# Kernel tuning notes

Measured on AMD Instinct MI355X. Metric: run time of the kernel, lower is better.

The kernel has to match this reference:

```python
import jax, jax.numpy as jnp
import numpy as np

B, HQ, HKV, D = 32, 32, 8, 128
PAGE = 16           # page_size == kv_seq_blk_size
PPS = 256           # pages per sequence -> 4096-token KV context
NPAGES = B * PPS


def setup_inputs() -> dict:
    key = jax.random.key(0)
    k1, k2, k3, k4 = jax.random.split(key, 4)
    q = jax.random.normal(k1, (B, HQ, 1, D), dtype=jnp.float32)
    paged_kv_cache = jax.random.normal(k2, (NPAGES, 2, HKV, PAGE, D), dtype=jnp.float32)
    # Uniform pages-per-sequence CSR layout; pages scattered randomly in the pool.
    kv_page_indptr = (jnp.arange(B + 1, dtype=jnp.int32) * PPS)
    kv_page_indices = jax.random.permutation(k3, NPAGES).astype(jnp.int32)
    kv_last_page_len = jax.random.randint(k4, (B,), 1, PAGE + 1, dtype=jnp.int32)
    return {
        "q": q,
        "paged_kv_cache": paged_kv_cache,
        "kv_page_indptr": kv_page_indptr,
        "kv_page_indices": kv_page_indices,
        "kv_last_page_len": kv_last_page_len,
    }


def reference(q, paged_kv_cache, kv_page_indptr, kv_page_indices, kv_last_page_len):
    b, hq, _, d = q.shape
    hkv = paged_kv_cache.shape[2]
    page = paged_kv_cache.shape[3]
    pps = kv_page_indices.shape[0] // b          # uniform pages per sequence
    groups = hq // hkv
    scale = 1.0 / jnp.sqrt(jnp.asarray(d, dtype=q.dtype))

    # Gather each sequence's pages: [B, PPS] page ids -> [B, PPS, HKV, PAGE, D]
    idx = kv_page_indices.reshape(b, pps)
    k = paged_kv_cache[idx, 0]
    v = paged_kv_cache[idx, 1]
    # -> [B, HKV, PPS*PAGE, D]
    k = jnp.transpose(k, (0, 2, 1, 3, 4)).reshape(b, hkv, pps * page, d)
    v = jnp.transpose(v, (0, 2, 1, 3, 4)).reshape(b, hkv, pps * page, d)

    # Valid length per sequence: full pages except a truncated last page.
    eff_len = (pps - 1) * page + kv_last_page_len            # [B]
    pos = jnp.arange(pps * page)
    valid = pos[None, :] < eff_len[:, None]                  # [B, S]

    # GQA: q heads grouped over kv heads.
    qr = q.reshape(b, hkv, groups, d)
    scores = jnp.einsum("bhgd,bhsd->bhgs", qr, k) * scale    # [B,HKV,G,S]
    scores = jnp.where(valid[:, None, None, :], scores, -jnp.inf)
    weights = jax.nn.softmax(scores, axis=-1)
    out = jnp.einsum("bhgs,bhsd->bhgd", weights, v)          # [B,HKV,G,D]
    return out.reshape(b, hq, 1, d)
```

## Files before the change

### kernel.cpp

```cpp
#include <hip/hip_runtime.h>
#include <math.h>

#define BB   32
#define HQ   32
#define HKV  8
#define DD   128
#define PAGE 16
#define GRP  4

__device__ __forceinline__ void async_ld16(const float* g, float* l) {
    __builtin_amdgcn_global_load_lds(
        (__attribute__((address_space(1))) void*)(g),
        (__attribute__((address_space(3))) void*)(l),
        16, 0, 0);
}

__global__ __launch_bounds__(256) void paged_decode(
    const float* __restrict__ q,
    const float* __restrict__ kv,
    const int*  __restrict__ indptr,
    const int*  __restrict__ indices,
    const int*  __restrict__ lastlen,
    float* __restrict__ out)
{
    __shared__ __align__(16) float sK[2][PAGE * DD];
    __shared__ __align__(16) float sV[2][PAGE * DD];

    const int tid  = threadIdx.x;
    const int w    = tid >> 6;
    const int lane = tid & 63;
    const int r    = lane >> 2;
    const int sub  = lane & 3;

    const int b  = blockIdx.x >> 3;
    const int h  = blockIdx.x & 7;
    const int qh = h * GRP + w;

    const float* qb = q + (size_t)(b * HQ + qh) * DD;
    float4 qv[8];
#pragma unroll
    for (int i = 0; i < 8; ++i) {
        int c = (sub * 32 + 4 * r + 4 * i) & 127;
        qv[i] = *(const float4*)(qb + c);
    }

    const int start = indptr[b];
    const int np    = indptr[b + 1] - start;
    const int ll    = lastlen[b];

    {
        const int pid0 = indices[start];
        const float* base = kv + (size_t)pid0 * (2 * HKV * PAGE * DD) + h * (PAGE * DD);
        const int c0 = w * 2;
        async_ld16(base + c0 * 256 + lane * 4,                 &sK[0][c0 * 256]);
        async_ld16(base + c0 * 256 + 256 + lane * 4,           &sK[0][c0 * 256 + 256]);
        async_ld16(base + HKV * PAGE * DD + c0 * 256 + lane * 4,       &sV[0][c0 * 256]);
        async_ld16(base + HKV * PAGE * DD + c0 * 256 + 256 + lane * 4, &sV[0][c0 * 256 + 256]);
    }
    int pid_next = (np > 1) ? indices[start + 1] : 0;

    float m = -INFINITY;
    float l = 0.0f;
    float ox = 0.0f, oy = 0.0f;
    const float scale = 0.08838834764831845f;

    for (int j = 0; j < np; ++j) {
        __syncthreads();
        const int buf = j & 1;

        if (j + 1 < np) {
            const float* base = kv + (size_t)pid_next * (2 * HKV * PAGE * DD) + h * (PAGE * DD);
            const int c0 = w * 2;
            float* kb = &sK[buf ^ 1][0];
            float* vb = &sV[buf ^ 1][0];
            async_ld16(base + c0 * 256 + lane * 4,                 kb + c0 * 256);
            async_ld16(base + c0 * 256 + 256 + lane * 4,           kb + c0 * 256 + 256);
            async_ld16(base + HKV * PAGE * DD + c0 * 256 + lane * 4,       vb + c0 * 256);
            async_ld16(base + HKV * PAGE * DD + c0 * 256 + 256 + lane * 4, vb + c0 * 256 + 256);
        }
        pid_next = (j + 2 < np) ? indices[start + j + 2] : 0;

        const float* Kb = sK[buf];
        const float* Vb = sV[buf];

        float acc = 0.0f;
#pragma unroll
        for (int i = 0; i < 8; ++i) {
            int c = (sub * 32 + 4 * r + 4 * i) & 127;
            float4 k4 = *(const float4*)(Kb + r * DD + c);
            acc += k4.x * qv[i].x + k4.y * qv[i].y + k4.z * qv[i].z + k4.w * qv[i].w;
        }
        acc += __shfl_xor(acc, 1, 64);
        acc += __shfl_xor(acc, 2, 64);
        float s = acc * scale;
        if ((j == np - 1) && (r >= ll)) s = -INFINITY;

        float pm = s;
        pm = fmaxf(pm, __shfl_xor(pm, 4, 64));
        pm = fmaxf(pm, __shfl_xor(pm, 8, 64));
        pm = fmaxf(pm, __shfl_xor(pm, 16, 64));
        pm = fmaxf(pm, __shfl_xor(pm, 32, 64));
        const float m_new = fmaxf(m, pm);
        const float p     = __expf(s - m_new);
        const float alpha = __expf(m - m_new);
        m = m_new;

        float ps = p;
        ps += __shfl_xor(ps, 4, 64);
        ps += __shfl_xor(ps, 8, 64);
        ps += __shfl_xor(ps, 16, 64);
        ps += __shfl_xor(ps, 32, 64);
        l = l * alpha + ps;

        ox *= alpha; oy *= alpha;
        const float* vrow = Vb + lane * 2;
#pragma unroll
        for (int rr = 0; rr < 16; ++rr) {
            float pr = __shfl(p, rr * 4, 64);
            float2 v2 = *(const float2*)(vrow + rr * DD);
            ox += pr * v2.x;
            oy += pr * v2.y;
        }
    }

    const float inv = 1.0f / l;
    float2 res; res.x = ox * inv; res.y = oy * inv;
    *(float2*)(out + (size_t)(b * HQ + qh) * DD + lane * 2) = res;
}

extern "C" void kernel_launch(void* const* d_in, const int* in_sizes, int n_in,
                              void* d_out, int out_size, void* d_ws, size_t ws_size,
                              hipStream_t stream) {
    const float* q       = (const float*)d_in[0];
    const float* kv      = (const float*)d_in[1];
    const int*   indptr  = (const int*)d_in[2];
    const int*   indices = (const int*)d_in[3];
    const int*   lastlen = (const int*)d_in[4];
    float* out = (float*)d_out;

    dim3 grid(BB * HKV);
    dim3 block(256);
    hipLaunchKernelGGL(paged_decode, grid, block, 0, stream,
                       q, kv, indptr, indices, lastlen, out);
}
```

Measured before the change: 1.485 ms.

## Split KV sequence across blocks with a combine kernel (flash-decoding)

Each (batch, kv-head) block's page range is split into 8 chunks, each handled by its own block that writes unnormalized partial output plus max and sum to workspace. A second kernel merges the partials with log-sum-exp rescaling. This raises the grid from 256 blocks to 2048 so more CUs are busy on a latency-bound decode, at the cost of a second launch and extra workspace traffic. Empty splits write neutral partials.

New measurement: 1.330 ms. 1.12x faster.

```diff
diff --git a/kernel.cpp b/kernel.cpp
--- a/kernel.cpp
+++ b/kernel.cpp
@@ -1,12 +1,14 @@
 #include <hip/hip_runtime.h>
 #include <math.h>
 
-#define BB   32
-#define HQ   32
-#define HKV  8
-#define DD   128
-#define PAGE 16
-#define GRP  4
+#define BB    32
+#define HQ    32
+#define HKV   8
+#define DD    128
+#define PAGE  16
+#define GRP   4
+#define SPLIT 8
+#define PSTR  130
 
 __device__ __forceinline__ void async_ld16(const float* g, float* l) {
     __builtin_amdgcn_global_load_lds(
@@ -15,13 +17,13 @@
         16, 0, 0);
 }
 
-__global__ __launch_bounds__(256) void paged_decode(
+__global__ __launch_bounds__(256) void paged_decode_split(
     const float* __restrict__ q,
     const float* __restrict__ kv,
     const int*  __restrict__ indptr,
     const int*  __restrict__ indices,
     const int*  __restrict__ lastlen,
-    float* __restrict__ out)
+    float* __restrict__ ws)
 {
     __shared__ __align__(16) float sK[2][PAGE * DD];
     __shared__ __align__(16) float sV[2][PAGE * DD];
@@ -32,8 +34,9 @@
     const int r    = lane >> 2;
     const int sub  = lane & 3;
 
-    const int b  = blockIdx.x >> 3;
-    const int h  = blockIdx.x & 7;
+    const int sp = blockIdx.x & 7;
+    const int h  = (blockIdx.x >> 3) & 7;
+    const int b  = blockIdx.x >> 6;
     const int qh = h * GRP + w;
 
     const float* qb = q + (size_t)(b * HQ + qh) * DD;
@@ -47,9 +50,21 @@
     const int start = indptr[b];
     const int np    = indptr[b + 1] - start;
     const int ll    = lastlen[b];
+    const int npp   = (np + SPLIT - 1) / SPLIT;
+    const int j0    = sp * npp;
+    const int j1    = (j0 + npp < np) ? (j0 + npp) : np;
+
+    float* P = ws + ((size_t)(b * HQ + qh) * SPLIT + sp) * PSTR;
+
+    if (j0 >= j1) {
+        float2 z; z.x = 0.0f; z.y = 0.0f;
+        *(float2*)(P + 2 * lane) = z;
+        if (lane == 0) { P[128] = -INFINITY; P[129] = 0.0f; }
+        return;
+    }
 
     {
-        const int pid0 = indices[start];
+        const int pid0 = indices[start + j0];
         const float* base = kv + (size_t)pid0 * (2 * HKV * PAGE * DD) + h * (PAGE * DD);
         const int c0 = w * 2;
         async_ld16(base + c0 * 256 + lane * 4,                 &sK[0][c0 * 256]);
@@ -57,18 +72,18 @@
         async_ld16(base + HKV * PAGE * DD + c0 * 256 + lane * 4,       &sV[0][c0 * 256]);
         async_ld16(base + HKV * PAGE * DD + c0 * 256 + 256 + lane * 4, &sV[0][c0 * 256 + 256]);
     }
-    int pid_next = (np > 1) ? indices[start + 1] : 0;
+    int pid_next = (j0 + 1 < j1) ? indices[start + j0 + 1] : 0;
 
     float m = -INFINITY;
     float l = 0.0f;
     float ox = 0.0f, oy = 0.0f;
     const float scale = 0.08838834764831845f;
 
-    for (int j = 0; j < np; ++j) {
+    for (int j = j0; j < j1; ++j) {
         __syncthreads();
-        const int buf = j & 1;
+        const int buf = (j - j0) & 1;
 
-        if (j + 1 < np) {
+        if (j + 1 < j1) {
             const float* base = kv + (size_t)pid_next * (2 * HKV * PAGE * DD) + h * (PAGE * DD);
             const int c0 = w * 2;
             float* kb = &sK[buf ^ 1][0];
@@ -78,7 +93,7 @@
             async_ld16(base + HKV * PAGE * DD + c0 * 256 + lane * 4,       vb + c0 * 256);
             async_ld16(base + HKV * PAGE * DD + c0 * 256 + 256 + lane * 4, vb + c0 * 256 + 256);
         }
-        pid_next = (j + 2 < np) ? indices[start + j + 2] : 0;
+        pid_next = (j + 2 < j1) ? indices[start + j + 2] : 0;
 
         const float* Kb = sK[buf];
         const float* Vb = sV[buf];
@@ -123,9 +138,39 @@
         }
     }
 
-    const float inv = 1.0f / l;
-    float2 res; res.x = ox * inv; res.y = oy * inv;
-    *(float2*)(out + (size_t)(b * HQ + qh) * DD + lane * 2) = res;
+    float2 res; res.x = ox; res.y = oy;
+    *(float2*)(P + 2 * lane) = res;
+    if (lane == 0) { P[128] = m; P[129] = l; }
+}
+
+__global__ __launch_bounds__(64) void paged_decode_combine(
+    const float* __restrict__ ws,
+    float* __restrict__ out)
+{
+    const int bh   = blockIdx.x;
+    const int lane = threadIdx.x;
+    const float* P = ws + (size_t)bh * SPLIT * PSTR;
+
+    float ms[SPLIT], ls[SPLIT];
+    float M = -INFINITY;
+#pragma unroll
+    for (int s = 0; s < SPLIT; ++s) {
+        ms[s] = P[s * PSTR + 128];
+        ls[s] = P[s * PSTR + 129];
+        M = fmaxf(M, ms[s]);
+    }
+    float L = 0.0f, ox = 0.0f, oy = 0.0f;
+#pragma unroll
+    for (int s = 0; s < SPLIT; ++s) {
+        const float a = __expf(ms[s] - M);
+        L += ls[s] * a;
+        float2 o2 = *(const float2*)(P + s * PSTR + 2 * lane);
+        ox += a * o2.x;
+        oy += a * o2.y;
+    }
+    const float inv = 1.0f / L;
+    float2 r; r.x = ox * inv; r.y = oy * inv;
+    *(float2*)(out + (size_t)bh * DD + 2 * lane) = r;
 }
 
 extern "C" void kernel_launch(void* const* d_in, const int* in_sizes, int n_in,
@@ -137,9 +182,18 @@
     const int*   indices = (const int*)d_in[3];
     const int*   lastlen = (const int*)d_in[4];
     float* out = (float*)d_out;
+    float* ws  = (float*)d_ws;
 
-    dim3 grid(BB * HKV);
-    dim3 block(256);
-    hipLaunchKernelGGL(paged_decode, grid, block, 0, stream,
-                       q, kv, indptr, indices, lastlen, out);
+    {
+        dim3 grid(BB * HKV * SPLIT);
+        dim3 block(256);
+        hipLaunchKernelGGL(paged_decode_split, grid, block, 0, stream,
+                           q, kv, indptr, indices, lastlen, ws);
+    }
+    {
+        dim3 grid(BB * HQ);
+        dim3 block(64);
+        hipLaunchKernelGGL(paged_decode_combine, grid, block, 0, stream,
+                           ws, out);
+    }
 }
```
